# Kernel optimization log

Hardware: AMD Instinct MI355X
Metric: run time of the kernel (lower is better)

## Reference

```python
import jax, jax.numpy as jnp
import numpy as np

N_NODES = 50000
N_EDGES = 640000
IN_CH = 128
HID_CH = 256


def setup_inputs() -> dict:
    key = jax.random.key(0)
    k_x, k_e, k_wl, k_bl, k_wr = jax.random.split(key, 5)
    x = jax.random.normal(k_x, (N_NODES, IN_CH), dtype=jnp.float32)
    edge_index = jax.random.randint(k_e, (2, N_EDGES), 0, N_NODES, dtype=jnp.int64)
    # PyG SAGEConv params: lin_l (applied to aggregated neighbors, with bias),
    # lin_r (root/self weight, no bias). Glorot-ish init scale.
    s = 1.0 / np.sqrt(IN_CH)
    W_l = jax.random.uniform(k_wl, (IN_CH, HID_CH), jnp.float32, -s, s)
    b_l = jnp.zeros((HID_CH,), dtype=jnp.float32)
    W_r = jax.random.uniform(k_wr, (IN_CH, HID_CH), jnp.float32, -s, s)
    return {"x": x, "edge_index": edge_index, "W_l": W_l, "b_l": b_l, "W_r": W_r}


def reference(x, edge_index, W_l, b_l, W_r):
    src, dst = edge_index[0], edge_index[1]
    # Gather source-node features per edge and mean-aggregate onto targets.
    msgs = x[src]                                            # [E, in]
    agg = jax.ops.segment_sum(msgs, dst, num_segments=N_NODES)   # [N, in]
    cnt = jax.ops.segment_sum(jnp.ones((N_EDGES,), x.dtype), dst,
                              num_segments=N_NODES)          # [N]
    mean = agg / jnp.maximum(cnt, 1.0)[:, None]
    # out = lin_l(mean_neighbors) + lin_r(x)
    return mean @ W_l + b_l + x @ W_r
```

## Files before the change

kernel.cpp:

```cpp
#include <hip/hip_runtime.h>


constexpr int N_NODES = 50000;
constexpr int N_EDGES = 640000;
constexpr int GEMM_TILES = (N_NODES + 127) / 128;
constexpr int CAP = 64;

constexpr int SCAT_BLOCKS  = N_EDGES / 1024;
constexpr int PREPX_BLOCKS = N_NODES * 32 / 256;
constexpr int WPREP_BLOCKS = 256;

typedef __attribute__((ext_vector_type(8))) short short8;
typedef __attribute__((ext_vector_type(4))) float f32x4;
typedef __attribute__((ext_vector_type(2))) float f32x2;
typedef _Float16 half8 __attribute__((ext_vector_type(8)));

__device__ inline unsigned short f2h(float f) {
    _Float16 h = (_Float16)f;
    return __builtin_bit_cast(unsigned short, h);
}

__global__ __launch_bounds__(256) void prep_k(const float* __restrict__ x,
                                              const int* __restrict__ ei,
                                              const float* __restrict__ Wl,
                                              const float* __restrict__ Wr,
                                              unsigned int* __restrict__ Abf_u,
                                              unsigned short* __restrict__ Wimg,
                                              int* __restrict__ cnt,
                                              int* __restrict__ slots,
                                              unsigned int* __restrict__ Xf8_u) {
    int bid = blockIdx.x, tid = threadIdx.x;
    if (bid < SCAT_BLOCKS) {
        int base = bid * 1024 + tid;
#pragma unroll
        for (int k = 0; k < 4; k++) {
            int e   = base + k * 256;
            int src = ei[e];
            int dst = ei[N_EDGES + e];
            int pos = atomicAdd(&cnt[dst], 1);
            if (pos < CAP) slots[(size_t)dst * CAP + pos] = src;
        }
    } else if (bid < SCAT_BLOCKS + PREPX_BLOCKS) {
        int t = (bid - SCAT_BLOCKS) * 256 + tid;
        float4 v = reinterpret_cast<const float4*>(x)[t];
        unsigned int p0 = (unsigned int)f2h(v.x) | ((unsigned int)f2h(v.y) << 16);
        unsigned int p1 = (unsigned int)f2h(v.z) | ((unsigned int)f2h(v.w) << 16);
        int row = t >> 5, c = t & 31;
        reinterpret_cast<uint2*>(Abf_u)[(size_t)row * 64 + 32 + c] =
            make_uint2(p0, p1);
        int u8 = __builtin_amdgcn_cvt_pk_fp8_f32(v.x, v.y, 0, false);
        u8     = __builtin_amdgcn_cvt_pk_fp8_f32(v.z, v.w, u8, true);
        Xf8_u[t] = (unsigned int)u8;
    } else {
        int t = (bid - SCAT_BLOCKS - PREPX_BLOCKS) * 256 + tid;
        int k = t >> 8, n = t & 255;
        float v = (k < 128) ? Wl[k * 256 + n] : Wr[(k - 128) * 256 + n];
        Wimg[(size_t)(k >> 5) * 8192 + n * 32 + (k & 31)] = f2h(v);
    }
}

__global__ __launch_bounds__(256) void agg_k(const int* __restrict__ cnt,
                                             const int* __restrict__ slots,
                                             const unsigned int* __restrict__ Xf8_u,
                                             unsigned int* __restrict__ Abf_u) {
    int wave = (blockIdx.x * 256 + threadIdx.x) >> 6;
    int lane = threadIdx.x & 63;
    int g    = lane >> 3;
    int sub  = lane & 7;
    int node = wave * 8 + g;
    if (node >= N_NODES) return;
    int dc   = cnt[node];
    int deg  = (dc > CAP) ? CAP : dc;
    const int* sl = slots + (size_t)node * CAP;
    const uint4* X8 = reinterpret_cast<const uint4*>(Xf8_u);

    f32x2 a0 = {0.f, 0.f}, a1 = {0.f, 0.f}, a2 = {0.f, 0.f}, a3 = {0.f, 0.f};
    f32x2 a4 = {0.f, 0.f}, a5 = {0.f, 0.f}, a6 = {0.f, 0.f}, a7 = {0.f, 0.f};

#define LOADV(vj, J)                                                    \
    uint4 vj = make_uint4(0, 0, 0, 0);                                  \
    {                                                                   \
        int sj = __shfl(slv, (J), 8);                                   \
        if (base + (J) < deg)                                           \
            vj = X8[(size_t)sj * 8 + sub];                              \
    }
#define ACCV(vj)                                                              \
    {                                                                         \
        a0 += __builtin_amdgcn_cvt_pk_f32_fp8(vj.x, false);                   \
        a1 += __builtin_amdgcn_cvt_pk_f32_fp8(vj.x, true);                    \
        a2 += __builtin_amdgcn_cvt_pk_f32_fp8(vj.y, false);                   \
        a3 += __builtin_amdgcn_cvt_pk_f32_fp8(vj.y, true);                    \
        a4 += __builtin_amdgcn_cvt_pk_f32_fp8(vj.z, false);                   \
        a5 += __builtin_amdgcn_cvt_pk_f32_fp8(vj.z, true);                    \
        a6 += __builtin_amdgcn_cvt_pk_f32_fp8(vj.w, false);                   \
        a7 += __builtin_amdgcn_cvt_pk_f32_fp8(vj.w, true);                    \
    }

    for (int base = 0; base < deg; base += 8) {
        int slv = sl[base + sub];
        LOADV(v0, 0) LOADV(v1, 1) LOADV(v2, 2) LOADV(v3, 3)
        LOADV(v4, 4) LOADV(v5, 5) LOADV(v6, 6) LOADV(v7, 7)
        ACCV(v0) ACCV(v1) ACCV(v2) ACCV(v3)
        ACCV(v4) ACCV(v5) ACCV(v6) ACCV(v7)
    }
#undef LOADV
#undef ACCV

    float inv = (dc > 0) ? 1.0f / (float)dc : 0.0f;
    uint4 o0, o1;
    o0.x = (unsigned int)f2h(a0.x * inv) | ((unsigned int)f2h(a0.y * inv) << 16);
    o0.y = (unsigned int)f2h(a1.x * inv) | ((unsigned int)f2h(a1.y * inv) << 16);
    o0.z = (unsigned int)f2h(a2.x * inv) | ((unsigned int)f2h(a2.y * inv) << 16);
    o0.w = (unsigned int)f2h(a3.x * inv) | ((unsigned int)f2h(a3.y * inv) << 16);
    o1.x = (unsigned int)f2h(a4.x * inv) | ((unsigned int)f2h(a4.y * inv) << 16);
    o1.y = (unsigned int)f2h(a5.x * inv) | ((unsigned int)f2h(a5.y * inv) << 16);
    o1.z = (unsigned int)f2h(a6.x * inv) | ((unsigned int)f2h(a6.y * inv) << 16);
    o1.w = (unsigned int)f2h(a7.x * inv) | ((unsigned int)f2h(a7.y * inv) << 16);
    uint4* A4 = reinterpret_cast<uint4*>(Abf_u);
    A4[(size_t)node * 32 + sub * 2]     = o0;
    A4[(size_t)node * 32 + sub * 2 + 1] = o1;
}

__global__ __launch_bounds__(512) void gemm_k(const unsigned short* __restrict__ Abf,
                                              const unsigned short* __restrict__ Wimg,
                                              const float* __restrict__ bl,
                                              float* __restrict__ out) {
    __shared__ unsigned short As[128 * 256];

    int tid  = threadIdx.x;
    int w8   = tid >> 6;
    int wm   = w8 >> 2;
    int wn   = w8 & 3;
    int lane = tid & 63;
    int m15  = lane & 15;
    int quad = lane >> 4;
    int bm   = blockIdx.x * 128;

    {
        int row = tid >> 2, q = tid & 3;
        int grow = bm + row;
        int r7 = row & 7;
#pragma unroll
        for (int kc = 0; kc < 8; kc++) {
            short8 v = {0, 0, 0, 0, 0, 0, 0, 0};
            if (grow < N_NODES)
                v = *reinterpret_cast<const short8*>(
                        Abf + (size_t)grow * 256 + kc * 32 + q * 8);
            int chunk = (kc * 4 + q) ^ r7;
            *reinterpret_cast<short8*>(As + row * 256 + chunk * 8) = v;
        }
    }
    __syncthreads();

    f32x4 zero4 = {0.f, 0.f, 0.f, 0.f};
    f32x4 acc[4][4];
#pragma unroll
    for (int rt = 0; rt < 4; rt++)
#pragma unroll
        for (int ct = 0; ct < 4; ct++) acc[rt][ct] = zero4;

    const unsigned short* Bbase =
        Wimg + ((size_t)(wn * 64 + m15) * 32 + quad * 8);

#pragma unroll
    for (int kc = 0; kc < 8; kc++) {
        half8 Af[4], Bf[4];
#pragma unroll
        for (int ct = 0; ct < 4; ct++)
            Bf[ct] = *reinterpret_cast<const half8*>(
                         Bbase + (size_t)kc * 8192 + ct * 512);
#pragma unroll
        for (int rt = 0; rt < 4; rt++) {
            int r = wm * 64 + rt * 16 + m15;
            int chunk = (kc * 4 + quad) ^ (r & 7);
            Af[rt] = *reinterpret_cast<const half8*>(As + r * 256 + chunk * 8);
        }
#pragma unroll
        for (int rt = 0; rt < 4; rt++)
#pragma unroll
            for (int ct = 0; ct < 4; ct++)
                acc[rt][ct] = __builtin_amdgcn_mfma_f32_16x16x32_f16(
                    Af[rt], Bf[ct], acc[rt][ct], 0, 0, 0);
    }

    float bias[4];
#pragma unroll
    for (int ct = 0; ct < 4; ct++) bias[ct] = bl[wn * 64 + ct * 16 + m15];
#pragma unroll
    for (int rt = 0; rt < 4; rt++) {
        int rb = bm + wm * 64 + rt * 16 + quad * 4;
#pragma unroll
        for (int r = 0; r < 4; r++) {
            int row = rb + r;
            if (row < N_NODES) {
#pragma unroll
                for (int ct = 0; ct < 4; ct++)
                    out[(size_t)row * 256 + wn * 64 + ct * 16 + m15] =
                        acc[rt][ct][r] + bias[ct];
            }
        }
    }
}

extern "C" void kernel_launch(void* const* d_in, const int* in_sizes, int n_in,
                              void* d_out, int out_size, void* d_ws, size_t ws_size,
                              hipStream_t stream) {
    const float* x  = (const float*)d_in[0];
    const int*   ei = (const int*)d_in[1];
    const float* Wl = (const float*)d_in[2];
    const float* bl = (const float*)d_in[3];
    const float* Wr = (const float*)d_in[4];
    float* out = (float*)d_out;

    unsigned short* Abf  = (unsigned short*)d_ws;
    unsigned short* Wimg = Abf + (size_t)N_NODES * 256;
    int* cnt   = (int*)(Wimg + 65536);
    int* slots = cnt + N_NODES;
    unsigned int* Xf8 = (unsigned int*)(slots + (size_t)N_NODES * CAP);

    hipMemsetAsync(cnt, 0, N_NODES * sizeof(int), stream);

    prep_k<<<SCAT_BLOCKS + PREPX_BLOCKS + WPREP_BLOCKS, 256, 0, stream>>>(
        x, ei, Wl, Wr, (unsigned int*)Abf, Wimg, cnt, slots, Xf8);
    agg_k<<<(N_NODES / 8 * 64 + 255) / 256, 256, 0, stream>>>(
        cnt, slots, Xf8, (unsigned int*)Abf);
    gemm_k<<<GEMM_TILES, 512, 0, stream>>>(Abf, Wimg, bl, out);
}
```

Measured before the change: 160.6 us.

## Fuse neighbor aggregation into GEMM kernel, writing means directly to LDS

```diff
diff --git a/kernel.cpp b/kernel.cpp
--- a/kernel.cpp
+++ b/kernel.cpp
@@ -19,6 +19,7 @@
     _Float16 h = (_Float16)f;
     return __builtin_bit_cast(unsigned short, h);
 }
+__device__ inline _Float16 f2hh(float f) { return (_Float16)f; }
 
 __global__ __launch_bounds__(256) void prep_k(const float* __restrict__ x,
                                               const int* __restrict__ ei,
@@ -59,23 +60,41 @@
     }
 }
 
-__global__ __launch_bounds__(256) void agg_k(const int* __restrict__ cnt,
-                                             const int* __restrict__ slots,
-                                             const unsigned int* __restrict__ Xf8_u,
-                                             unsigned int* __restrict__ Abf_u) {
-    int wave = (blockIdx.x * 256 + threadIdx.x) >> 6;
-    int lane = threadIdx.x & 63;
+__global__ __launch_bounds__(512) void aggemm_k(const int* __restrict__ cnt,
+                                                const int* __restrict__ slots,
+                                                const unsigned int* __restrict__ Xf8_u,
+                                                const unsigned short* __restrict__ Abf,
+                                                const unsigned short* __restrict__ Wimg,
+                                                const float* __restrict__ bl,
+                                                float* __restrict__ out) {
+    __shared__ unsigned short As[128 * 256];
+
+    int tid  = threadIdx.x;
+    int w8   = tid >> 6;
+    int wm   = w8 >> 2;
+    int wn   = w8 & 3;
+    int lane = tid & 63;
+    int m15  = lane & 15;
+    int quad = lane >> 4;
     int g    = lane >> 3;
     int sub  = lane & 7;
-    int node = wave * 8 + g;
-    if (node >= N_NODES) return;
-    int dc   = cnt[node];
-    int deg  = (dc > CAP) ? CAP : dc;
-    const int* sl = slots + (size_t)node * CAP;
+    int bm   = blockIdx.x * 128;
+
     const uint4* X8 = reinterpret_cast<const uint4*>(Xf8_u);
 
-    f32x2 a0 = {0.f, 0.f}, a1 = {0.f, 0.f}, a2 = {0.f, 0.f}, a3 = {0.f, 0.f};
-    f32x2 a4 = {0.f, 0.f}, a5 = {0.f, 0.f}, a6 = {0.f, 0.f}, a7 = {0.f, 0.f};
+#pragma unroll 1
+    for (int round = 0; round < 2; round++) {
+        int r_ofs = w8 * 16 + round * 8 + g;
+        int node  = bm + r_ofs;
+        int dc = 0, deg = 0;
+        if (node < N_NODES) {
+            dc  = cnt[node];
+            deg = (dc > CAP) ? CAP : dc;
+        }
+        const int* sl = slots + (size_t)node * CAP;
+
+        f32x2 a0 = {0.f, 0.f}, a1 = {0.f, 0.f}, a2 = {0.f, 0.f}, a3 = {0.f, 0.f};
+        f32x2 a4 = {0.f, 0.f}, a5 = {0.f, 0.f}, a6 = {0.f, 0.f}, a7 = {0.f, 0.f};
 
 #define LOADV(vj, J)                                                    \
     uint4 vj = make_uint4(0, 0, 0, 0);                                  \
@@ -96,52 +115,38 @@
         a7 += __builtin_amdgcn_cvt_pk_f32_fp8(vj.w, true);                    \
     }
 
-    for (int base = 0; base < deg; base += 8) {
-        int slv = sl[base + sub];
-        LOADV(v0, 0) LOADV(v1, 1) LOADV(v2, 2) LOADV(v3, 3)
-        LOADV(v4, 4) LOADV(v5, 5) LOADV(v6, 6) LOADV(v7, 7)
-        ACCV(v0) ACCV(v1) ACCV(v2) ACCV(v3)
-        ACCV(v4) ACCV(v5) ACCV(v6) ACCV(v7)
-    }
+        for (int base = 0; base < deg; base += 8) {
+            int slv = (base + sub < deg) ? sl[base + sub] : 0;
+            LOADV(v0, 0) LOADV(v1, 1) LOADV(v2, 2) LOADV(v3, 3)
+            LOADV(v4, 4) LOADV(v5, 5) LOADV(v6, 6) LOADV(v7, 7)
+            ACCV(v0) ACCV(v1) ACCV(v2) ACCV(v3)
+            ACCV(v4) ACCV(v5) ACCV(v6) ACCV(v7)
+        }
 #undef LOADV
 #undef ACCV
 
-    float inv = (dc > 0) ? 1.0f / (float)dc : 0.0f;
-    uint4 o0, o1;
-    o0.x = (unsigned int)f2h(a0.x * inv) | ((unsigned int)f2h(a0.y * inv) << 16);
-    o0.y = (unsigned int)f2h(a1.x * inv) | ((unsigned int)f2h(a1.y * inv) << 16);
-    o0.z = (unsigned int)f2h(a2.x * inv) | ((unsigned int)f2h(a2.y * inv) << 16);
-    o0.w = (unsigned int)f2h(a3.x * inv) | ((unsigned int)f2h(a3.y * inv) << 16);
-    o1.x = (unsigned int)f2h(a4.x * inv) | ((unsigned int)f2h(a4.y * inv) << 16);
-    o1.y = (unsigned int)f2h(a5.x * inv) | ((unsigned int)f2h(a5.y * inv) << 16);
-    o1.z = (unsigned int)f2h(a6.x * inv) | ((unsigned int)f2h(a6.y * inv) << 16);
-    o1.w = (unsigned int)f2h(a7.x * inv) | ((unsigned int)f2h(a7.y * inv) << 16);
-    uint4* A4 = reinterpret_cast<uint4*>(Abf_u);
-    A4[(size_t)node * 32 + sub * 2]     = o0;
-    A4[(size_t)node * 32 + sub * 2 + 1] = o1;
-}
-
-__global__ __launch_bounds__(512) void gemm_k(const unsigned short* __restrict__ Abf,
-                                              const unsigned short* __restrict__ Wimg,
-                                              const float* __restrict__ bl,
-                                              float* __restrict__ out) {
-    __shared__ unsigned short As[128 * 256];
-
-    int tid  = threadIdx.x;
-    int w8   = tid >> 6;
-    int wm   = w8 >> 2;
-    int wn   = w8 & 3;
-    int lane = tid & 63;
-    int m15  = lane & 15;
-    int quad = lane >> 4;
-    int bm   = blockIdx.x * 128;
+        float inv = (dc > 0) ? 1.0f / (float)dc : 0.0f;
+        half8 h0, h1;
+        h0[0] = f2hh(a0.x * inv); h0[1] = f2hh(a0.y * inv);
+        h0[2] = f2hh(a1.x * inv); h0[3] = f2hh(a1.y * inv);
+        h0[4] = f2hh(a2.x * inv); h0[5] = f2hh(a2.y * inv);
+        h0[6] = f2hh(a3.x * inv); h0[7] = f2hh(a3.y * inv);
+        h1[0] = f2hh(a4.x * inv); h1[1] = f2hh(a4.y * inv);
+        h1[2] = f2hh(a5.x * inv); h1[3] = f2hh(a5.y * inv);
+        h1[4] = f2hh(a6.x * inv); h1[5] = f2hh(a6.y * inv);
+        h1[6] = f2hh(a7.x * inv); h1[7] = f2hh(a7.y * inv);
+        int r7 = r_ofs & 7;
+        int c0 = 2 * sub, c1 = 2 * sub + 1;
+        *reinterpret_cast<half8*>(As + r_ofs * 256 + (c0 ^ r7) * 8) = h0;
+        *reinterpret_cast<half8*>(As + r_ofs * 256 + (c1 ^ r7) * 8) = h1;
+    }
 
     {
         int row = tid >> 2, q = tid & 3;
         int grow = bm + row;
         int r7 = row & 7;
 #pragma unroll
-        for (int kc = 0; kc < 8; kc++) {
+        for (int kc = 4; kc < 8; kc++) {
             short8 v = {0, 0, 0, 0, 0, 0, 0, 0};
             if (grow < N_NODES)
                 v = *reinterpret_cast<const short8*>(
@@ -222,7 +227,6 @@
 
     prep_k<<<SCAT_BLOCKS + PREPX_BLOCKS + WPREP_BLOCKS, 256, 0, stream>>>(
         x, ei, Wl, Wr, (unsigned int*)Abf, Wimg, cnt, slots, Xf8);
-    agg_k<<<(N_NODES / 8 * 64 + 255) / 256, 256, 0, stream>>>(
-        cnt, slots, Xf8, (unsigned int*)Abf);
-    gemm_k<<<GEMM_TILES, 512, 0, stream>>>(Abf, Wimg, bl, out);
-}
+    aggemm_k<<<GEMM_TILES, 512, 0, stream>>>(cnt, slots, Xf8, Abf, Wimg, bl,
+                                             out);
+}
```

Measured after the change: 150.7 us. -6.1%, faster.
